# Optimization experiments

Measured on AMD Instinct MI355X. Metric: run time of the kernel, lower is better.

Reference implementation:

```python
import jax, jax.numpy as jnp
import numpy as np


def _sobel_filters():
    # 3D Sobel kernels for x, y, z directions, shape (3, 1, 3, 3, 3) in OIDHW.
    x = np.array([[[-1, 0, 1], [-2, 0, 2], [-1, 0, 1]],
                  [[-2, 0, 2], [-4, 0, 4], [-2, 0, 2]],
                  [[-1, 0, 1], [-2, 0, 2], [-1, 0, 1]]], dtype=np.float32)
    y = np.array([[[1, 2, 1], [0, 0, 0], [-1, -2, -1]],
                  [[2, 4, 2], [0, 0, 0], [-2, -4, -2]],
                  [[1, 2, 1], [0, 0, 0], [-1, -2, -1]]], dtype=np.float32)
    z = np.array([[[1, 2, 1], [2, 4, 2], [1, 2, 1]],
                  [[0, 0, 0], [0, 0, 0], [0, 0, 0]],
                  [[-1, -2, -1], [-2, -4, -2], [-1, -2, -1]]], dtype=np.float32)
    return jnp.asarray(np.stack([x, y, z])[:, None])  # (3,1,3,3,3)


_FILTERS = _sobel_filters()
_EPS = 1e-10


def gradient3d(x):
    # x: [B,1,D,H,W] -> gradient magnitude [B,1,D,H,W].
    # Single conv with 3 output channels == three separate torch conv3d + concat.
    g = jax.lax.conv_general_dilated(
        x, _FILTERS, window_strides=(1, 1, 1),
        padding=[(1, 1), (1, 1), (1, 1)],
        dimension_numbers=('NCDHW', 'OIDHW', 'NCDHW'))  # [B,3,D,H,W]
    return jnp.sqrt(jnp.sum(g * g, axis=1, keepdims=True) + _EPS)


def setup_inputs() -> dict:
    key = jax.random.key(0)
    k1, k2, k3 = jax.random.split(key, 3)
    shape = (2, 1, 192, 192, 192)
    pred = jax.random.normal(k1, shape, dtype=jnp.float32)
    gt_dose = jax.random.normal(k2, shape, dtype=jnp.float32)
    body_mask = (jax.random.uniform(k3, shape) > 0.3).astype(jnp.float32)
    return {"pred": pred, "gt_dose": gt_dose, "body_mask": body_mask}


def reference(pred, gt_dose, body_mask):
    mse = jnp.square(pred - gt_dose) * body_mask
    mge = jnp.square(gradient3d(gt_dose) - gradient3d(pred)) * body_mask
    return jnp.mean(mse + jnp.tanh(mge) * mse)
```

## Files before the change

kernel.cpp:

```cpp
#include <hip/hip_runtime.h>
#include <math.h>

#define W 192
#define H 192
#define DEPTH 192
#define BATCH 2
#define TW 64
#define TH 8
#define DC 12
#define HW (H * W)
#define VOL ((size_t)DEPTH * HW)
#define NPAIR 7
#define LROW 128
#define LPL (10 * LROW)
#define NUNIT 640


__global__ __launch_bounds__(256) void sobel_loss_part(
    const float* __restrict__ pred, const float* __restrict__ gt,
    const float* __restrict__ mask, float* __restrict__ partials)
{
    __shared__ __align__(16) float lds[4 * LPL];

    const int tid = threadIdx.x;
    const int tx = blockIdx.x % 3, ty = blockIdx.x / 3;
    const int w0 = tx * TW, h0 = ty * TH;
    const int d0 = blockIdx.y * DC;
    const size_t base = (size_t)blockIdx.z * VOL;

    const int wy  = tid >> 5;
    const int wxo = (tid & 31) << 1;
    const size_t coff = base + (size_t)(h0 + wy) * W + (w0 + wxo);

    int u_st[3], u_rowok[3], u_lok[3], u_rok[3], u_q[3], u_lds[3];
    size_t u_goff[3];
    const float* u_src[3];
    #pragma unroll
    for (int k = 0; k < 3; ++k) {
        int u = tid + 256 * k;
        int uu = (u < NUNIT) ? u : 0;
        int a = uu / 320; int rem = uu - a * 320;
        int q = rem / 160; int rem2 = rem - q * 160;
        int r = rem2 >> 4; int cg = rem2 & 15;
        int y = h0 - 1 + r;
        int x = w0 + 4 * cg;
        u_st[k]    = (u < NUNIT);
        u_rowok[k] = u_st[k] && ((unsigned)y < (unsigned)H);
        u_lok[k]   = (x > 0);
        u_rok[k]   = (x + 4 < W);
        u_goff[k]  = u_rowok[k] ? ((size_t)y * W + x) : 0;
        u_q[k]     = q;
        u_lds[k]   = ((a * 2 + q) * 10 + r) * LROW + cg * 8;
        u_src[k]   = a ? gt : pred;
    }

    float4 X[3]; float XL[3], XR[3];
    auto load_pair = [&](int s) {
        const int p0 = d0 - 1 + 2 * s;
        #pragma unroll
        for (int k = 0; k < 3; ++k) {
            const int p = p0 + u_q[k];
            const bool ok = u_rowok[k] && (p >= 0) && (p < DEPTH);
            const float* sp = u_src[k] + base + (size_t)p * HW + u_goff[k];
            X[k]  = ok ? *(const float4*)sp : make_float4(0.f, 0.f, 0.f, 0.f);
            XL[k] = (ok && u_lok[k]) ? sp[-1] : 0.f;
            XR[k] = (ok && u_rok[k]) ? sp[4]  : 0.f;
        }
    };

    float2 Mn = {0,0}, Mn1 = {0,0}, Pn = {0,0}, Pn1 = {0,0}, Gn = {0,0}, Gn1 = {0,0};
    auto load_ctr = [&](int s) {
        size_t o0 = coff + (size_t)(d0 + 2 * s - 2) * HW;
        size_t o1 = coff + (size_t)(d0 + 2 * s - 1) * HW;
        Mn  = *(const float2*)(mask + o0);  Mn1 = *(const float2*)(mask + o1);
        Pn  = *(const float2*)(pred + o0);  Pn1 = *(const float2*)(pred + o1);
        Gn  = *(const float2*)(gt   + o0);  Gn1 = *(const float2*)(gt   + o1);
    };

    float hdx[2][2][3], hsx[2][2][3], hdy[2][2][3];
    #pragma unroll
    for (int a = 0; a < 2; ++a)
        #pragma unroll
        for (int o = 0; o < 2; ++o)
            #pragma unroll
            for (int j = 0; j < 3; ++j) { hdx[a][o][j] = 0.f; hsx[a][o][j] = 0.f; hdy[a][o][j] = 0.f; }
    float acc = 0.f;

    load_pair(0);

    #pragma unroll
    for (int s = 0; s < NPAIR; ++s) {
        __syncthreads();
        #pragma unroll
        for (int k = 0; k < 3; ++k) {
            if (u_st[k]) {
                float4 x4 = X[k]; float xl = XL[k], xr = XR[k];
                float4 w1, w2;
                w1.x = xl   + 2.f * x4.x + x4.y;  w1.y = x4.y - xl;
                w1.z = x4.x + 2.f * x4.y + x4.z;  w1.w = x4.z - x4.x;
                w2.x = x4.y + 2.f * x4.z + x4.w;  w2.y = x4.w - x4.y;
                w2.z = x4.z + 2.f * x4.w + xr;    w2.w = xr   - x4.z;
                *(float4*)(lds + u_lds[k])     = w1;
                *(float4*)(lds + u_lds[k] + 4) = w2;
            }
        }
        __syncthreads();

        float2 Mc0 = Mn, Mc1 = Mn1, Pc0 = Pn, Pc1 = Pn1, Gc0 = Gn, Gc1 = Gn1;
        if (s + 1 < NPAIR) { load_pair(s + 1); load_ctr(s + 1); }

        #pragma unroll
        for (int q = 0; q < 2; ++q) {
            const int t = 2 * s + q;
            const int wsl = t % 3;
            const int i0  = (t + 1) % 3;
            const int i1  = (t + 2) % 3;
            const int i2  = wsl;

            const float* LA = lds + (q * 10 + wy) * LROW + wxo * 2;
            const float* LB = lds + ((2 + q) * 10 + wy) * LROW + wxo * 2;
            float4 A0 = *(const float4*)(LA);
            float4 A1 = *(const float4*)(LA + LROW);
            float4 A2 = *(const float4*)(LA + 2 * LROW);
            float4 B0 = *(const float4*)(LB);
            float4 B1 = *(const float4*)(LB + LROW);
            float4 B2 = *(const float4*)(LB + 2 * LROW);

            #pragma unroll
            for (int o = 0; o < 2; ++o) {
                float sA0 = o ? A0.z : A0.x, dA0 = o ? A0.w : A0.y;
                float sA1 = o ? A1.z : A1.x, dA1 = o ? A1.w : A1.y;
                float sA2 = o ? A2.z : A2.x, dA2 = o ? A2.w : A2.y;
                hdx[0][o][wsl] = dA0 + 2.f * dA1 + dA2;
                hsx[0][o][wsl] = sA0 + 2.f * sA1 + sA2;
                hdy[0][o][wsl] = sA0 - sA2;
                float sB0 = o ? B0.z : B0.x, dB0 = o ? B0.w : B0.y;
                float sB1 = o ? B1.z : B1.x, dB1 = o ? B1.w : B1.y;
                float sB2 = o ? B2.z : B2.x, dB2 = o ? B2.w : B2.y;
                hdx[1][o][wsl] = dB0 + 2.f * dB1 + dB2;
                hsx[1][o][wsl] = sB0 + 2.f * sB1 + sB2;
                hdy[1][o][wsl] = sB0 - sB2;
            }

            if (t >= 2) {
                const float2 M = q ? Mc1 : Mc0;
                const float2 P = q ? Pc1 : Pc0;
                const float2 G = q ? Gc1 : Gc0;
                #pragma unroll
                for (int o = 0; o < 2; ++o) {
                    float gx = hdx[0][o][i0] + 2.f * hdx[0][o][i1] + hdx[0][o][i2];
                    float gy = hdy[0][o][i0] + 2.f * hdy[0][o][i1] + hdy[0][o][i2];
                    float gz = hsx[0][o][i0] - hsx[0][o][i2];
                    float ga = __builtin_amdgcn_sqrtf(
                        fmaf(gz, gz, fmaf(gy, gy, fmaf(gx, gx, 1e-10f))));
                    float hx = hdx[1][o][i0] + 2.f * hdx[1][o][i1] + hdx[1][o][i2];
                    float hy = hdy[1][o][i0] + 2.f * hdy[1][o][i1] + hdy[1][o][i2];
                    float hz = hsx[1][o][i0] - hsx[1][o][i2];
                    float gb = __builtin_amdgcn_sqrtf(
                        fmaf(hz, hz, fmaf(hy, hy, fmaf(hx, hx, 1e-10f))));
                    float m  = o ? M.y : M.x;
                    float dm = (o ? P.y : P.x) - (o ? G.y : G.x);
                    float mse = dm * dm * m;
                    float dg  = gb - ga;
                    float mge = dg * dg * m;
                    float ex = __expf(mge + mge);
                    float rc = __builtin_amdgcn_rcpf(ex + 1.f);
                    float c  = fmaf(-2.f, rc, 2.f);
                    acc = fmaf(mse, c, acc);
                }
            }
        }
    }

    float v = acc;
    #pragma unroll
    for (int o = 32; o > 0; o >>= 1) v += __shfl_down(v, o, 64);
    __shared__ float red[4];
    if ((tid & 63) == 0) red[tid >> 6] = v;
    __syncthreads();
    if (tid == 0) {
        partials[(size_t)blockIdx.z * (gridDim.x * gridDim.y)
                 + (size_t)blockIdx.y * gridDim.x + blockIdx.x]
            = red[0] + red[1] + red[2] + red[3];
    }
}

__global__ __launch_bounds__(256) void reduce_final(
    const float* __restrict__ partials, int n, float* __restrict__ out)
{
    int tid = threadIdx.x;
    double s = 0.0;
    for (int i = tid; i < n; i += 256) s += (double)partials[i];
    #pragma unroll
    for (int o = 32; o > 0; o >>= 1) s += __shfl_down(s, o, 64);
    __shared__ double red[4];
    if ((tid & 63) == 0) red[tid >> 6] = s;
    __syncthreads();
    if (tid == 0) {
        double t = red[0] + red[1] + red[2] + red[3];
        const double ntot = (double)BATCH * (double)DEPTH * (double)H * (double)W;
        out[0] = (float)(t / ntot);
    }
}

extern "C" void kernel_launch(void* const* d_in, const int* in_sizes, int n_in,
                              void* d_out, int out_size, void* d_ws, size_t ws_size,
                              hipStream_t stream) {
    const float* pred = (const float*)d_in[0];
    const float* gt   = (const float*)d_in[1];
    const float* mask = (const float*)d_in[2];
    float* partials = (float*)d_ws;

    dim3 grid((W / TW) * (H / TH), DEPTH / DC, BATCH);
    sobel_loss_part<<<grid, 256, 0, stream>>>(pred, gt, mask, partials);

    int nparts = grid.x * grid.y * grid.z;
    reduce_final<<<1, 256, 0, stream>>>(partials, nparts, (float*)d_out);
}
```

Before: 186.6 us.

## Stage raw planes in double-buffered LDS, one plane per round

The kernel now copies raw input rows, including 4-wide halo columns, into a double-buffered LDS area one depth plane per round. It no longer precomputes the horizontal Sobel partials in registers and stores them two planes at a time. Each thread reads six float2 values per row and does the x-direction smoothing and difference itself. This needs one barrier per plane instead of two per plane pair, and it drops the scalar halo loads. The cost is more LDS reads and ALU work per output, more rounds (14 instead of 7) with smaller overlap windows, and possible LDS bank conflicts from the row stride of 72.

```diff
diff --git a/kernel.cpp b/kernel.cpp
--- a/kernel.cpp
+++ b/kernel.cpp
@@ -10,17 +10,17 @@
 #define DC 12
 #define HW (H * W)
 #define VOL ((size_t)DEPTH * HW)
-#define NPAIR 7
-#define LROW 128
+#define ROUNDS (DC + 2)
+#define LROW 72
 #define LPL (10 * LROW)
-#define NUNIT 640
+#define NUNIT 360
 
 
 __global__ __launch_bounds__(256) void sobel_loss_part(
     const float* __restrict__ pred, const float* __restrict__ gt,
     const float* __restrict__ mask, float* __restrict__ partials)
 {
-    __shared__ __align__(16) float lds[4 * LPL];
+    __shared__ __align__(16) float lds[2 * 2 * LPL];
 
     const int tid = threadIdx.x;
     const int tx = blockIdx.x % 3, ty = blockIdx.x / 3;
@@ -30,51 +30,43 @@
 
     const int wy  = tid >> 5;
     const int wxo = (tid & 31) << 1;
-    const size_t coff = base + (size_t)(h0 + wy) * W + (w0 + wxo);
+    const int ctr_off = (h0 + wy) * W + (w0 + wxo);
 
-    int u_st[3], u_rowok[3], u_lok[3], u_rok[3], u_q[3], u_lds[3];
-    size_t u_goff[3];
-    const float* u_src[3];
+    int s_ld[2], s_go[2], s_a[2];
+    bool s_row[2];
     #pragma unroll
-    for (int k = 0; k < 3; ++k) {
+    for (int k = 0; k < 2; ++k) {
         int u = tid + 256 * k;
         int uu = (u < NUNIT) ? u : 0;
-        int a = uu / 320; int rem = uu - a * 320;
-        int q = rem / 160; int rem2 = rem - q * 160;
-        int r = rem2 >> 4; int cg = rem2 & 15;
+        int a = uu / 180; int rem = uu - a * 180;
+        int r = rem / 18; int cg = rem - r * 18;
         int y = h0 - 1 + r;
-        int x = w0 + 4 * cg;
-        u_st[k]    = (u < NUNIT);
-        u_rowok[k] = u_st[k] && ((unsigned)y < (unsigned)H);
-        u_lok[k]   = (x > 0);
-        u_rok[k]   = (x + 4 < W);
-        u_goff[k]  = u_rowok[k] ? ((size_t)y * W + x) : 0;
-        u_q[k]     = q;
-        u_lds[k]   = ((a * 2 + q) * 10 + r) * LROW + cg * 8;
-        u_src[k]   = a ? gt : pred;
+        int x = w0 - 4 + 4 * cg;
+        bool rok = (u < NUNIT) && ((unsigned)y < (unsigned)H) && ((unsigned)x < (unsigned)W);
+        s_row[k] = rok;
+        s_go[k]  = rok ? (y * W + x) : 0;
+        s_ld[k]  = (a * 10 + r) * LROW + 4 * cg;
+        s_a[k]   = a;
     }
 
-    float4 X[3]; float XL[3], XR[3];
-    auto load_pair = [&](int s) {
-        const int p0 = d0 - 1 + 2 * s;
+    float4 X[2];
+    auto load_plane = [&](int p) {
+        const bool pv = (p >= 0) && (p < DEPTH);
+        const size_t pb = base + (size_t)(pv ? p : 0) * HW;
         #pragma unroll
-        for (int k = 0; k < 3; ++k) {
-            const int p = p0 + u_q[k];
-            const bool ok = u_rowok[k] && (p >= 0) && (p < DEPTH);
-            const float* sp = u_src[k] + base + (size_t)p * HW + u_goff[k];
-            X[k]  = ok ? *(const float4*)sp : make_float4(0.f, 0.f, 0.f, 0.f);
-            XL[k] = (ok && u_lok[k]) ? sp[-1] : 0.f;
-            XR[k] = (ok && u_rok[k]) ? sp[4]  : 0.f;
+        for (int k = 0; k < 2; ++k) {
+            const bool ok = pv && s_row[k];
+            const float* sp = (s_a[k] ? gt : pred) + pb + s_go[k];
+            X[k] = ok ? *(const float4*)sp : make_float4(0.f, 0.f, 0.f, 0.f);
         }
     };
 
-    float2 Mn = {0,0}, Mn1 = {0,0}, Pn = {0,0}, Pn1 = {0,0}, Gn = {0,0}, Gn1 = {0,0};
-    auto load_ctr = [&](int s) {
-        size_t o0 = coff + (size_t)(d0 + 2 * s - 2) * HW;
-        size_t o1 = coff + (size_t)(d0 + 2 * s - 1) * HW;
-        Mn  = *(const float2*)(mask + o0);  Mn1 = *(const float2*)(mask + o1);
-        Pn  = *(const float2*)(pred + o0);  Pn1 = *(const float2*)(pred + o1);
-        Gn  = *(const float2*)(gt   + o0);  Gn1 = *(const float2*)(gt   + o1);
+    float2 Mn = {0,0}, Pn = {0,0}, Gn = {0,0};
+    auto load_ctr = [&](int od) {
+        const size_t o = base + (size_t)od * HW + ctr_off;
+        Mn = *(const float2*)(mask + o);
+        Pn = *(const float2*)(pred + o);
+        Gn = *(const float2*)(gt   + o);
     };
 
     float hdx[2][2][3], hsx[2][2][3], hdy[2][2][3];
@@ -83,91 +75,67 @@
         #pragma unroll
         for (int o = 0; o < 2; ++o)
             #pragma unroll
-            for (int j = 0; j < 3; ++j) { hdx[a][o][j] = 0.f; hsx[a][o][j] = 0.f; hdy[a][o][j] = 0.f; }
+            for (int j = 0; j < 3; ++j) { hdx[a][o][j]=0.f; hsx[a][o][j]=0.f; hdy[a][o][j]=0.f; }
     float acc = 0.f;
+    float2 Mc, Pc, Gc;
 
-    load_pair(0);
+    load_plane(d0 - 1);
 
     #pragma unroll
-    for (int s = 0; s < NPAIR; ++s) {
+    for (int t = 0; t < ROUNDS; ++t) {
+        const int buf = t & 1;
+        *(float4*)(lds + buf * 2 * LPL + s_ld[0]) = X[0];
+        if (tid < NUNIT - 256)
+            *(float4*)(lds + buf * 2 * LPL + s_ld[1]) = X[1];
         __syncthreads();
+
+        if (t + 1 < ROUNDS) load_plane(d0 + t);
+        Mc = Mn; Pc = Pn; Gc = Gn;
+        if (t >= 1 && t <= DC) load_ctr(d0 + t - 1);
+
+        const int wsl = t % 3;
+        const int i0  = (t + 1) % 3;
+        const int i1  = (t + 2) % 3;
+
         #pragma unroll
-        for (int k = 0; k < 3; ++k) {
-            if (u_st[k]) {
-                float4 x4 = X[k]; float xl = XL[k], xr = XR[k];
-                float4 w1, w2;
-                w1.x = xl   + 2.f * x4.x + x4.y;  w1.y = x4.y - xl;
-                w1.z = x4.x + 2.f * x4.y + x4.z;  w1.w = x4.z - x4.x;
-                w2.x = x4.y + 2.f * x4.z + x4.w;  w2.y = x4.w - x4.y;
-                w2.z = x4.z + 2.f * x4.w + xr;    w2.w = xr   - x4.z;
-                *(float4*)(lds + u_lds[k])     = w1;
-                *(float4*)(lds + u_lds[k] + 4) = w2;
+        for (int a = 0; a < 2; ++a) {
+            const float* R = lds + (buf * 2 + a) * LPL + wy * LROW + (wxo + 2);
+            float2 v00 = *(const float2*)(R),            v01 = *(const float2*)(R + 2),            v02 = *(const float2*)(R + 4);
+            float2 v10 = *(const float2*)(R + LROW),     v11 = *(const float2*)(R + LROW + 2),     v12 = *(const float2*)(R + LROW + 4);
+            float2 v20 = *(const float2*)(R + 2*LROW),   v21 = *(const float2*)(R + 2*LROW + 2),   v22 = *(const float2*)(R + 2*LROW + 4);
+            #pragma unroll
+            for (int o = 0; o < 2; ++o) {
+                float sh0 = o ? (v01.x + 2.f*v01.y + v02.x) : (v00.y + 2.f*v01.x + v01.y);
+                float dh0 = o ? (v02.x - v01.x)             : (v01.y - v00.y);
+                float sh1 = o ? (v11.x + 2.f*v11.y + v12.x) : (v10.y + 2.f*v11.x + v11.y);
+                float dh1 = o ? (v12.x - v11.x)             : (v11.y - v10.y);
+                float sh2 = o ? (v21.x + 2.f*v21.y + v22.x) : (v20.y + 2.f*v21.x + v21.y);
+                float dh2 = o ? (v22.x - v21.x)             : (v21.y - v20.y);
+                hdx[a][o][wsl] = dh0 + 2.f * dh1 + dh2;
+                hsx[a][o][wsl] = sh0 + 2.f * sh1 + sh2;
+                hdy[a][o][wsl] = sh0 - sh2;
             }
         }
-        __syncthreads();
 
-        float2 Mc0 = Mn, Mc1 = Mn1, Pc0 = Pn, Pc1 = Pn1, Gc0 = Gn, Gc1 = Gn1;
-        if (s + 1 < NPAIR) { load_pair(s + 1); load_ctr(s + 1); }
-
-        #pragma unroll
-        for (int q = 0; q < 2; ++q) {
-            const int t = 2 * s + q;
-            const int wsl = t % 3;
-            const int i0  = (t + 1) % 3;
-            const int i1  = (t + 2) % 3;
-            const int i2  = wsl;
-
-            const float* LA = lds + (q * 10 + wy) * LROW + wxo * 2;
-            const float* LB = lds + ((2 + q) * 10 + wy) * LROW + wxo * 2;
-            float4 A0 = *(const float4*)(LA);
-            float4 A1 = *(const float4*)(LA + LROW);
-            float4 A2 = *(const float4*)(LA + 2 * LROW);
-            float4 B0 = *(const float4*)(LB);
-            float4 B1 = *(const float4*)(LB + LROW);
-            float4 B2 = *(const float4*)(LB + 2 * LROW);
-
+        if (t >= 2) {
             #pragma unroll
             for (int o = 0; o < 2; ++o) {
-                float sA0 = o ? A0.z : A0.x, dA0 = o ? A0.w : A0.y;
-                float sA1 = o ? A1.z : A1.x, dA1 = o ? A1.w : A1.y;
-                float sA2 = o ? A2.z : A2.x, dA2 = o ? A2.w : A2.y;
-                hdx[0][o][wsl] = dA0 + 2.f * dA1 + dA2;
-                hsx[0][o][wsl] = sA0 + 2.f * sA1 + sA2;
-                hdy[0][o][wsl] = sA0 - sA2;
-                float sB0 = o ? B0.z : B0.x, dB0 = o ? B0.w : B0.y;
-                float sB1 = o ? B1.z : B1.x, dB1 = o ? B1.w : B1.y;
-                float sB2 = o ? B2.z : B2.x, dB2 = o ? B2.w : B2.y;
-                hdx[1][o][wsl] = dB0 + 2.f * dB1 + dB2;
-                hsx[1][o][wsl] = sB0 + 2.f * sB1 + sB2;
-                hdy[1][o][wsl] = sB0 - sB2;
-            }
-
-            if (t >= 2) {
-                const float2 M = q ? Mc1 : Mc0;
-                const float2 P = q ? Pc1 : Pc0;
-                const float2 G = q ? Gc1 : Gc0;
-                #pragma unroll
-                for (int o = 0; o < 2; ++o) {
-                    float gx = hdx[0][o][i0] + 2.f * hdx[0][o][i1] + hdx[0][o][i2];
-                    float gy = hdy[0][o][i0] + 2.f * hdy[0][o][i1] + hdy[0][o][i2];
-                    float gz = hsx[0][o][i0] - hsx[0][o][i2];
-                    float ga = __builtin_amdgcn_sqrtf(
-                        fmaf(gz, gz, fmaf(gy, gy, fmaf(gx, gx, 1e-10f))));
-                    float hx = hdx[1][o][i0] + 2.f * hdx[1][o][i1] + hdx[1][o][i2];
-                    float hy = hdy[1][o][i0] + 2.f * hdy[1][o][i1] + hdy[1][o][i2];
-                    float hz = hsx[1][o][i0] - hsx[1][o][i2];
-                    float gb = __builtin_amdgcn_sqrtf(
-                        fmaf(hz, hz, fmaf(hy, hy, fmaf(hx, hx, 1e-10f))));
-                    float m  = o ? M.y : M.x;
-                    float dm = (o ? P.y : P.x) - (o ? G.y : G.x);
-                    float mse = dm * dm * m;
-                    float dg  = gb - ga;
-                    float mge = dg * dg * m;
-                    float ex = __expf(mge + mge);
-                    float rc = __builtin_amdgcn_rcpf(ex + 1.f);
-                    float c  = fmaf(-2.f, rc, 2.f);
-                    acc = fmaf(mse, c, acc);
-                }
+                float gx = hdx[0][o][i0] + 2.f * hdx[0][o][i1] + hdx[0][o][wsl];
+                float gy = hdy[0][o][i0] + 2.f * hdy[0][o][i1] + hdy[0][o][wsl];
+                float gz = hsx[0][o][i0] - hsx[0][o][wsl];
+                float ga = __builtin_amdgcn_sqrtf(fmaf(gz, gz, fmaf(gy, gy, fmaf(gx, gx, 1e-10f))));
+                float hx = hdx[1][o][i0] + 2.f * hdx[1][o][i1] + hdx[1][o][wsl];
+                float hy = hdy[1][o][i0] + 2.f * hdy[1][o][i1] + hdy[1][o][wsl];
+                float hz = hsx[1][o][i0] - hsx[1][o][wsl];
+                float gb = __builtin_amdgcn_sqrtf(fmaf(hz, hz, fmaf(hy, hy, fmaf(hx, hx, 1e-10f))));
+                float m  = o ? Mc.y : Mc.x;
+                float dm = (o ? Pc.y : Pc.x) - (o ? Gc.y : Gc.x);
+                float mse = dm * dm * m;
+                float dg  = gb - ga;
+                float mge = dg * dg * m;
+                float ex = __expf(mge + mge);
+                float rc = __builtin_amdgcn_rcpf(ex + 1.f);
+                acc = fmaf(mse, fmaf(-2.f, rc, 2.f), acc);
             }
         }
     }
```

After: 260.9 us. +39.8%, slower.
